# Kernel optimization log

Hardware: AMD Instinct MI355X
Metric: run time of the kernel (lower is better)

Reference implementation:

```python
import jax, jax.numpy as jnp
import numpy as np

B, R, N, D, H, QK, K = 32, 200, 200, 128, 8, 16, 10
CLIP = 10.0  # standard POMO logit clipping


def setup_inputs() -> dict:
    key = jax.random.key(0)
    ks = jax.random.split(key, 12)
    encoded_nodes = jax.random.normal(ks[0], (B, N, D), jnp.float32)
    distance = jax.random.uniform(ks[1], (B, N, N), jnp.float32)
    current = jax.random.randint(ks[2], (B, R), 0, N)
    u = jax.random.uniform(ks[3], (B, R, N))
    ninf_mask = jnp.where(u < 0.3, -jnp.inf, 0.0).astype(jnp.float32)
    s = 0.02
    Wq = jax.random.normal(ks[4], (2 * D, H * QK), jnp.float32) * s
    Wk = jax.random.normal(ks[5], (D, H * QK), jnp.float32) * s
    Wv = jax.random.normal(ks[6], (D, H * QK), jnp.float32) * s
    Wmhc = jax.random.normal(ks[7], (H * QK, D), jnp.float32) * s
    b_mhc = jnp.zeros((D,), jnp.float32)
    W1 = jax.random.normal(ks[8], (K * D, 5 * D), jnp.float32) * s
    b1 = jnp.zeros((5 * D,), jnp.float32)
    W2 = jax.random.normal(ks[9], (5 * D, D), jnp.float32) * s
    b2 = jnp.zeros((D,), jnp.float32)
    return {"encoded_nodes": encoded_nodes, "distance": distance, "ninf_mask": ninf_mask,
            "current": current, "Wq": Wq, "Wk": Wk, "Wv": Wv, "Wmhc": Wmhc, "b_mhc": b_mhc,
            "W1": W1, "b1": b1, "W2": W2, "b2": b2}


def _search_unvisited(current, distance, ninf_mask):
    # rows of distance at current nodes: [B,R,N] (avoids B*R*N*N materialization)
    dist_f = jnp.take_along_axis(distance, current[:, :, None], axis=1)
    dist_m = jnp.where(jnp.isfinite(ninf_mask), dist_f, jnp.inf)
    neg_vals, idx = jax.lax.top_k(-dist_m, K)  # k smallest distances
    vals = -neg_vals
    return jnp.where(jnp.isinf(vals), N, idx)  # pad index N for masked-out slots


def _gather_pad0(encoded_nodes, idx):
    padded = jnp.concatenate([encoded_nodes, jnp.zeros((B, 1, D), encoded_nodes.dtype)], axis=1)
    g = jnp.take_along_axis(padded, idx.reshape(B, R * K)[:, :, None], axis=1)
    return g.reshape(B, R, K, D)


def _gather_pad_avg(a):
    # replace all-zero (pad) rows by the mean of non-zero rows within each [K,D] group
    is_zero = jnp.sum(a, axis=-1) == 0  # [B,R,K]
    cnt = jnp.maximum(jnp.sum(~is_zero, axis=-1).astype(a.dtype), 1e-9)  # [B,R]
    mean = jnp.sum(a, axis=2) / cnt[..., None]  # [B,R,D]
    return jnp.where(is_zero[..., None], mean[:, :, None, :], a)


def reference(encoded_nodes, distance, ninf_mask, current,
              Wq, Wk, Wv, Wmhc, b_mhc, W1, b1, W2, b2):
    knn = _search_unvisited(current, distance, ninf_mask)         # [B,R,K]
    a = _gather_pad0(encoded_nodes, knn)                          # [B,R,K,D]
    b = _gather_pad_avg(a)                                        # [B,R,K,D]
    h = jnp.maximum(b.reshape(B, R, K * D) @ W1 + b1, 0.0)
    unv = h @ W2 + b2                                             # [B,R,D]
    cur_emb = jnp.take_along_axis(encoded_nodes, current[:, :, None], axis=1)  # [B,R,D]
    qin = jnp.concatenate([cur_emb, unv], axis=-1)                # [B,R,2D]
    q = (qin @ Wq).reshape(B, R, H, QK).transpose(0, 2, 1, 3)     # [B,H,R,QK]
    k = (encoded_nodes @ Wk).reshape(B, N, H, QK).transpose(0, 2, 1, 3)
    v = (encoded_nodes @ Wv).reshape(B, N, H, QK).transpose(0, 2, 1, 3)
    score = jnp.einsum('bhrd,bhnd->bhrn', q, k) / jnp.sqrt(jnp.float32(QK))
    score = score + ninf_mask[:, None]                            # [B,H,R,N]
    w = jax.nn.softmax(score, axis=-1)
    out = jnp.einsum('bhrn,bhnd->bhrd', w, v)
    out = out.transpose(0, 2, 1, 3).reshape(B, R, H * QK)
    mh = out @ Wmhc + b_mhc                                       # [B,R,D]
    sh = jnp.einsum('brd,bnd->brn', mh, encoded_nodes) / jnp.sqrt(jnp.float32(D))
    logits = CLIP * jnp.tanh(sh) + ninf_mask
    return jax.nn.softmax(logits, axis=-1)                        # [B,R,N]
```

## Files before the change

kernel.cpp:

```cpp
#include <hip/hip_runtime.h>
#include <hip/hip_bf16.h>
#include <math.h>

#define Bc 32
#define Rc 200
#define Nc 200
#define Dc 128
#define Hc 8
#define QKc 16
#define Kc 10
#define BRc (Bc*Rc)

typedef __attribute__((ext_vector_type(8))) short short8;
typedef __attribute__((ext_vector_type(4))) float f32x4;
typedef unsigned long long u64;

#define GLOAD_LDS16(g, l) __builtin_amdgcn_global_load_lds( \
    (const __attribute__((address_space(1))) void*)(g), \
    (__attribute__((address_space(3))) void*)(l), 16, 0, 0)

__device__ inline void transpose_tile(const float* __restrict__ src, int lds_,
                                      __hip_bfloat16* __restrict__ dst, int ldd,
                                      int k0, int n0, float scale)
{
    __shared__ float tile[32][33];
    int tx = threadIdx.x & 31, ty = threadIdx.x >> 5;
    #pragma unroll
    for (int i = ty; i < 32; i += 8)
        tile[i][tx] = src[(size_t)(k0 + i) * lds_ + n0 + tx];
    __syncthreads();
    #pragma unroll
    for (int i = ty; i < 32; i += 8)
        dst[(size_t)(n0 + i) * ldd + k0 + tx] = __float2bfloat16(tile[tx][i] * scale);
}

__global__ __launch_bounds__(256) void prep_knn_kernel(
    const float* __restrict__ W1, const float* __restrict__ W2,
    const float* __restrict__ Wq, const float* __restrict__ Wmhc,
    const float* __restrict__ Wk, const float* __restrict__ Wv,
    const float* __restrict__ b2, const float* __restrict__ enc,
    const float* __restrict__ dist, const float* __restrict__ mask,
    const int* __restrict__ cur,
    __hip_bfloat16* __restrict__ W1t, __hip_bfloat16* __restrict__ Wkvt,
    __hip_bfloat16* __restrict__ Wmb, __hip_bfloat16* __restrict__ Wcat,
    float* __restrict__ bq, __hip_bfloat16* __restrict__ encb,
    unsigned* __restrict__ aoff, __hip_bfloat16* __restrict__ hq,
    u64* __restrict__ maskbits)
{
    int bid = blockIdx.x;
    int t = threadIdx.x;
    if (bid < 800) {
        transpose_tile(W1, 640, W1t, 1280, (bid % 40) * 32, (bid / 40) * 32, 1.f);
    } else if (bid < 816) {
        int id = bid - 800;
        transpose_tile(Wk, 128, Wkvt, 128, (id & 3) * 32, (id >> 2) * 32, 1.f);
    } else if (bid < 832) {
        int id = bid - 816;
        transpose_tile(Wv, 128, Wkvt + 128 * 128, 128, (id & 3) * 32, (id >> 2) * 32, 1.f);
    } else if (bid < 848) {
        int e = (bid - 832) * 1024 + t * 4;
        #pragma unroll
        for (int j = 0; j < 4; ++j) Wmb[e + j] = __float2bfloat16(Wmhc[e + j]);
    } else if (bid < 864) {
        int id = bid - 848;
        transpose_tile(Wq, 128, Wcat, 768, (id & 3) * 32, (id >> 2) * 32, 0.25f);
    } else if (bid < 904) {
        int j0 = (bid - 864) * 16;
        int n = t & 127, half = t >> 7;
        #pragma unroll
        for (int jj = 0; jj < 8; ++jj) {
            int j = j0 + half * 8 + jj;
            float acc = 0.f;
            for (int k = 0; k < 128; ++k)
                acc = fmaf(W2[(size_t)j * 128 + k], Wq[(size_t)(128 + k) * 128 + n], acc);
            Wcat[(size_t)n * 768 + 128 + j] = __float2bfloat16(acc * 0.25f);
        }
    } else if (bid < 929) {
        size_t base = (size_t)(bid - 904) * 32768 + (size_t)t * 4;
        #pragma unroll 4
        for (int it = 0; it < 32; ++it) {
            size_t i = base + (size_t)it * 1024;
            float4 v = *(const float4*)(enc + i);
            encb[i + 0] = __float2bfloat16(v.x);
            encb[i + 1] = __float2bfloat16(v.y);
            encb[i + 2] = __float2bfloat16(v.z);
            encb[i + 3] = __float2bfloat16(v.w);
        }
    } else if (bid == 929) {
        if (t < 128) {
            float acc = 0.f;
            for (int k = 0; k < 128; ++k)
                acc = fmaf(b2[k], Wq[(size_t)(128 + k) * 128 + t], acc);
            bq[t] = acc * 0.25f;
        }
    } else {
        int lane = t & 63, w = t >> 6;
        int br = (bid - 930) * 4 + w;
        int b = br / Rc;
        int c = cur[br];
        const float* drow = dist + ((size_t)b * Nc + c) * Nc;
        const float* mrow = mask + (size_t)br * Nc;

        float v[4];
        #pragma unroll
        for (int j = 0; j < 4; ++j) {
            int n = lane + 64 * j;
            bool allowed = false;
            float val = INFINITY;
            if (n < Nc) {
                float mv = mrow[n];
                if (!isinf(mv)) { val = drow[n]; allowed = true; }
            }
            v[j] = val;
            u64 wb = __ballot(allowed);
            if (lane == 0) maskbits[(size_t)br * 4 + j] = wb;
        }
        int idxs[Kc];
        unsigned myrow = 0;
        #pragma unroll
        for (int k = 0; k < Kc; ++k) {
            float bv = v[0]; int bn = lane;
            #pragma unroll
            for (int j = 1; j < 4; ++j) {
                if (v[j] < bv) { bv = v[j]; bn = lane + 64 * j; }
            }
            #pragma unroll
            for (int off = 32; off > 0; off >>= 1) {
                float ov = __shfl_xor(bv, off);
                int   on = __shfl_xor(bn, off);
                if (ov < bv || (ov == bv && on < bn)) { bv = ov; bn = on; }
            }
            bool pad = isinf(bv);
            idxs[k] = pad ? Nc : bn;
            if (lane == k) myrow = pad ? (unsigned)(Bc * Nc + br) : (unsigned)(b * Nc + bn);
            int oj = bn >> 6, ol = bn & 63;
            if (!pad && lane == ol) v[oj] = INFINITY;
        }
        if (lane < Kc) aoff[(size_t)br * 16 + lane] = myrow << 7;

        const float* erow = enc + ((size_t)b * Nc + c) * Dc;
        __hip_bfloat16* hrow = hq + (size_t)br * 768;
        hrow[lane]      = __float2bfloat16(erow[lane]);
        hrow[lane + 64] = __float2bfloat16(erow[lane + 64]);

        if (idxs[Kc - 1] == Nc) {
            float cnt = 0.f;
            #pragma unroll
            for (int k = 0; k < Kc; ++k) cnt += (idxs[k] < Nc) ? 1.f : 0.f;
            float icnt = 1.f / fmaxf(cnt, 1e-9f);
            #pragma unroll
            for (int half = 0; half < 2; ++half) {
                int d = lane + 64 * half;
                float sum = 0.f;
                #pragma unroll
                for (int k = 0; k < Kc; ++k) {
                    if (idxs[k] < Nc)
                        sum += enc[((size_t)b * Nc + idxs[k]) * Dc + d];
                }
                encb[((size_t)(Bc * Nc) + br) * Dc + d] = __float2bfloat16(sum * icnt);
            }
        }
    }
}

__global__ __launch_bounds__(256) void fused_gemms_kernel(
    const __hip_bfloat16* __restrict__ encb, const unsigned* __restrict__ aoff,
    const __hip_bfloat16* __restrict__ W1t, const float* __restrict__ b1,
    const __hip_bfloat16* __restrict__ Wkvt, const __hip_bfloat16* __restrict__ Wmb,
    const float* __restrict__ bmhc, const float* __restrict__ enc,
    __hip_bfloat16* __restrict__ hq, __hip_bfloat16* __restrict__ kvf,
    __hip_bfloat16* __restrict__ em, float* __restrict__ be)
{
    __shared__ short Asl[4][64 * 32];
    __shared__ short Bsl[4][64 * 32];
    int bid = blockIdx.x;
    int tid = threadIdx.x;
    int wave = tid >> 6, lane = tid & 63;
    int lrow = lane >> 2;
    int cg   = lane & 3;
    int ss   = (lane >> 3) & 3;
    int gq   = (cg - ss) & 3;
    int wm = wave >> 1, wn = wave & 1;
    int rrow = lane & 15, quad = lane >> 4;
    int srd  = (rrow >> 1) & 3;
    int strip = (wave & 1) * 32;

    if (bid < 1000) {
        int m0 = (bid / 10) * 64, n0 = (bid % 10) * 64;
        unsigned o0[Kc], o1[Kc];
        if (wave < 2) {
            const unsigned* ap0 = aoff + (size_t)(m0 + strip + lrow) * 16;
            const unsigned* ap1 = ap0 + 16 * 16;
            #pragma unroll
            for (int j = 0; j < Kc; ++j) { o0[j] = ap0[j]; o1[j] = ap1[j]; }
        }
        const short* Eb = (const short*)encb;
        const short* gB0 = (const short*)W1t + (size_t)(n0 + strip + lrow) * 1280 + gq * 8;
        const short* gB1 = gB0 + (size_t)16 * 1280;

        f32x4 acc[2][2];
        #pragma unroll
        for (int i = 0; i < 2; ++i)
            #pragma unroll
            for (int j = 0; j < 2; ++j)
                acc[i][j] = (f32x4){0.f, 0.f, 0.f, 0.f};

        #pragma unroll
        for (int kt = 0; kt < 10; ++kt) {
            __syncthreads();
            #pragma unroll
            for (int s = 0; s < 4; ++s) {
                if (wave < 2) {
                    GLOAD_LDS16(Eb + o0[kt] + s * 32 + gq * 8, &Asl[s][strip * 32]);
                    GLOAD_LDS16(Eb + o1[kt] + s * 32 + gq * 8, &Asl[s][(strip + 16) * 32]);
                } else {
                    GLOAD_LDS16(gB0 + kt * 128 + s * 32, &Bsl[s][strip * 32]);
                    GLOAD_LDS16(gB1 + kt * 128 + s * 32, &Bsl[s][(strip + 16) * 32]);
                }
            }
            __syncthreads();
            #pragma unroll
            for (int s = 0; s < 4; ++s) {
                short8 afr[2], bfr[2];
                #pragma unroll
                for (int mt = 0; mt < 2; ++mt)
                    afr[mt] = *(const short8*)&Asl[s][(wm * 32 + mt * 16 + rrow) * 32 + ((quad + srd) & 3) * 8];
                #pragma unroll
                for (int nt = 0; nt < 2; ++nt)
                    bfr[nt] = *(const short8*)&Bsl[s][(wn * 32 + nt * 16 + rrow) * 32 + ((quad + srd) & 3) * 8];
                #pragma unroll
                for (int mt = 0; mt < 2; ++mt)
                    #pragma unroll
                    for (int nt = 0; nt < 2; ++nt)
                        acc[mt][nt] = __builtin_amdgcn_mfma_f32_16x16x32_bf16(
                            afr[mt], bfr[nt], acc[mt][nt], 0, 0, 0);
            }
        }
        #pragma unroll
        for (int mt = 0; mt < 2; ++mt)
            #pragma unroll
            for (int nt = 0; nt < 2; ++nt) {
                int n = wn * 32 + nt * 16 + rrow;
                float bv = b1[n0 + n];
                #pragma unroll
                for (int i = 0; i < 4; ++i) {
                    int m = m0 + wm * 32 + mt * 16 + quad * 4 + i;
                    float vv = fmaxf(acc[mt][nt][i] + bv, 0.f);
                    hq[(size_t)m * 768 + 128 + n0 + n] = __float2bfloat16(vv);
                }
            }
    } else if (bid < 1600) {
        const short* Bbase; __hip_bfloat16* Cout; int ldc, m0, n0;
        if (bid < 1400) {
            int id = bid - 1000;
            Bbase = (const short*)Wkvt; Cout = kvf; ldc = 256;
            m0 = (id >> 2) * 64; n0 = (id & 3) * 64;
        } else {
            int id = bid - 1400;
            Bbase = (const short*)Wmb; Cout = em; ldc = 128;
            m0 = (id >> 1) * 64; n0 = (id & 1) * 64;
        }
        const short* g0 = (wave < 2)
            ? (const short*)encb + (size_t)(m0 + strip + lrow) * 128 + gq * 8
            : Bbase + (size_t)(n0 + strip + lrow) * 128 + gq * 8;
        const short* g1 = g0 + (size_t)16 * 128;

        f32x4 acc[2][2];
        #pragma unroll
        for (int i = 0; i < 2; ++i)
            #pragma unroll
            for (int j = 0; j < 2; ++j)
                acc[i][j] = (f32x4){0.f, 0.f, 0.f, 0.f};

        #pragma unroll
        for (int s = 0; s < 4; ++s) {
            short* l0 = (wave < 2) ? &Asl[s][strip * 32] : &Bsl[s][strip * 32];
            short* l1 = (wave < 2) ? &Asl[s][(strip + 16) * 32] : &Bsl[s][(strip + 16) * 32];
            GLOAD_LDS16(g0 + s * 32, l0);
            GLOAD_LDS16(g1 + s * 32, l1);
        }
        __syncthreads();
        #pragma unroll
        for (int s = 0; s < 4; ++s) {
            short8 afr[2], bfr[2];
            #pragma unroll
            for (int mt = 0; mt < 2; ++mt)
                afr[mt] = *(const short8*)&Asl[s][(wm * 32 + mt * 16 + rrow) * 32 + ((quad + srd) & 3) * 8];
            #pragma unroll
            for (int nt = 0; nt < 2; ++nt)
                bfr[nt] = *(const short8*)&Bsl[s][(wn * 32 + nt * 16 + rrow) * 32 + ((quad + srd) & 3) * 8];
            #pragma unroll
            for (int mt = 0; mt < 2; ++mt)
                #pragma unroll
                for (int nt = 0; nt < 2; ++nt)
                    acc[mt][nt] = __builtin_amdgcn_mfma_f32_16x16x32_bf16(
                        afr[mt], bfr[nt], acc[mt][nt], 0, 0, 0);
        }
        #pragma unroll
        for (int mt = 0; mt < 2; ++mt)
            #pragma unroll
            for (int nt = 0; nt < 2; ++nt) {
                int n = wn * 32 + nt * 16 + rrow;
                #pragma unroll
                for (int i = 0; i < 4; ++i) {
                    int m = m0 + wm * 32 + mt * 16 + quad * 4 + i;
                    Cout[(size_t)m * ldc + n0 + n] = __float2bfloat16(acc[mt][nt][i]);
                }
            }
    } else {
        int i = (bid - 1600) * 256 + tid;
        if (i < Bc * Nc) {
            const float* row = enc + (size_t)i * 128;
            float acc = 0.f;
            #pragma unroll
            for (int dq = 0; dq < 32; ++dq) {
                float4 e4 = *(const float4*)(row + dq * 4);
                acc = fmaf(bmhc[dq * 4 + 0], e4.x, acc);
                acc = fmaf(bmhc[dq * 4 + 1], e4.y, acc);
                acc = fmaf(bmhc[dq * 4 + 2], e4.z, acc);
                acc = fmaf(bmhc[dq * 4 + 3], e4.w, acc);
            }
            be[i] = acc;
        }
    }
}

__global__ __launch_bounds__(256) void qgemm_kernel(
    const __hip_bfloat16* __restrict__ hq, const __hip_bfloat16* __restrict__ Wcat,
    const float* __restrict__ bq, __hip_bfloat16* __restrict__ q)
{
    __shared__ short Asl[4][64 * 32];
    __shared__ short Bsl[4][64 * 32];
    int tid = threadIdx.x;
    int wave = tid >> 6, lane = tid & 63;
    int m0 = blockIdx.y * 64, n0 = blockIdx.x * 64;
    int lrow = lane >> 2;
    int cg   = lane & 3;
    int ss   = (lane >> 3) & 3;
    int gq   = (cg - ss) & 3;
    int wm = wave >> 1, wn = wave & 1;
    int rrow = lane & 15, quad = lane >> 4;
    int srd  = (rrow >> 1) & 3;
    int strip = (wave & 1) * 32;

    const short* g0 = (wave < 2)
        ? (const short*)hq + (size_t)(m0 + strip + lrow) * 768 + gq * 8
        : (const short*)Wcat + (size_t)(n0 + strip + lrow) * 768 + gq * 8;
    const short* g1 = g0 + (size_t)16 * 768;

    f32x4 acc[2][2];
    #pragma unroll
    for (int i = 0; i < 2; ++i)
        #pragma unroll
        for (int j = 0; j < 2; ++j)
            acc[i][j] = (f32x4){0.f, 0.f, 0.f, 0.f};

    for (int k0 = 0; k0 < 768; k0 += 128) {
        __syncthreads();
        #pragma unroll
        for (int s = 0; s < 4; ++s) {
            short* l0 = (wave < 2) ? &Asl[s][strip * 32] : &Bsl[s][strip * 32];
            short* l1 = (wave < 2) ? &Asl[s][(strip + 16) * 32] : &Bsl[s][(strip + 16) * 32];
            GLOAD_LDS16(g0 + k0 + s * 32, l0);
            GLOAD_LDS16(g1 + k0 + s * 32, l1);
        }
        __syncthreads();
        #pragma unroll
        for (int s = 0; s < 4; ++s) {
            short8 afr[2], bfr[2];
            #pragma unroll
            for (int mt = 0; mt < 2; ++mt)
                afr[mt] = *(const short8*)&Asl[s][(wm * 32 + mt * 16 + rrow) * 32 + ((quad + srd) & 3) * 8];
            #pragma unroll
            for (int nt = 0; nt < 2; ++nt)
                bfr[nt] = *(const short8*)&Bsl[s][(wn * 32 + nt * 16 + rrow) * 32 + ((quad + srd) & 3) * 8];
            #pragma unroll
            for (int mt = 0; mt < 2; ++mt)
                #pragma unroll
                for (int nt = 0; nt < 2; ++nt)
                    acc[mt][nt] = __builtin_amdgcn_mfma_f32_16x16x32_bf16(
                        afr[mt], bfr[nt], acc[mt][nt], 0, 0, 0);
        }
    }

    #pragma unroll
    for (int mt = 0; mt < 2; ++mt) {
        #pragma unroll
        for (int nt = 0; nt < 2; ++nt) {
            int n = wn * 32 + nt * 16 + rrow;
            float bv = bq[n0 + n];
            #pragma unroll
            for (int i = 0; i < 4; ++i) {
                int m = m0 + wm * 32 + mt * 16 + quad * 4 + i;
                q[(size_t)m * 128 + n0 + n] = __float2bfloat16(acc[mt][nt][i] + bv);
            }
        }
    }
}

__global__ __launch_bounds__(256) void attn_mfma_kernel(
    const __hip_bfloat16* __restrict__ q, const __hip_bfloat16* __restrict__ kvf,
    const u64* __restrict__ maskbits, __hip_bfloat16* __restrict__ att)
{
    constexpr int RP = 208;
    constexpr int QS = 40;
    constexpr int VS = 232;
    __shared__ short Qs[RP * QS];
    __shared__ short Ks[RP * QS];
    __shared__ short Vt[16 * VS];
    __shared__ short Ps[4][16 * VS];
    __shared__ u64 smask[RP][4];

    int b = blockIdx.x >> 3, h = blockIdx.x & 7;
    int half = blockIdx.y;
    int t = threadIdx.x;
    int wave = t >> 6, lane = t & 63;
    int rrow = lane & 15, quad = lane >> 4;

    const short8 z8 = {0, 0, 0, 0, 0, 0, 0, 0};
    for (int idx = t; idx < RP * 2; idx += 256) {
        int r = idx >> 1, g = idx & 1;
        short8 qa = z8, ka = z8;
        if (r < Rc) {
            qa = *(const short8*)((const short*)q + ((size_t)(b * Rc + r)) * 128 + h * 16 + g * 8);
            ka = *(const short8*)((const short*)kvf + ((size_t)(b * Nc + r)) * 256 + h * 16 + g * 8);
        }
        *(short8*)&Qs[r * QS + g * 8] = qa;
        *(short8*)&Ks[r * QS + g * 8] = ka;
        *(short8*)&Qs[r * QS + 16 + g * 8] = z8;
        *(short8*)&Ks[r * QS + 16 + g * 8] = z8;
    }
    if (t < Rc) {
        const short* vp = (const short*)kvf + ((size_t)(b * Nc + t)) * 256 + 128 + h * 16;
        short8 v0 = *(const short8*)vp;
        short8 v1 = *(const short8*)(vp + 8);
        #pragma unroll
        for (int d = 0; d < 8; ++d) Vt[d * VS + t] = v0[d];
        #pragma unroll
        for (int d = 0; d < 8; ++d) Vt[(d + 8) * VS + t] = v1[d];
    }
    for (int idx = t; idx < 16 * 32; idx += 256) {
        int d = idx >> 5, cN = 200 + (idx & 31);
        if (cN < VS) Vt[d * VS + cN] = 0;
    }
    for (int idx = lane; idx < 16 * 16; idx += 64) {
        int rr = idx >> 4, cc = 208 + (idx & 15);
        Ps[wave][rr * VS + cc] = 0;
    }
    for (int idx = t; idx < RP * 4; idx += 256) {
        int r = idx >> 2, w = idx & 3;
        smask[r][w] = (r < Rc) ? maskbits[((size_t)b * Rc + r) * 4 + w] : ~0ull;
    }
    __syncthreads();

    int rt0 = half * 7, rt1 = half ? 13 : 7;
    for (int rt = rt0 + wave; rt < rt1; rt += 4) {
        short8 qf = *(const short8*)&Qs[(rt * 16 + rrow) * QS + quad * 8];
        f32x4 sacc[13];
        #pragma unroll
        for (int nt = 0; nt < 13; ++nt) {
            short8 kf = *(const short8*)&Ks[(nt * 16 + rrow) * QS + quad * 8];
            sacc[nt] = __builtin_amdgcn_mfma_f32_16x16x32_bf16(
                qf, kf, (f32x4){0.f, 0.f, 0.f, 0.f}, 0, 0, 0);
        }
        float inv[4];
        #pragma unroll
        for (int i = 0; i < 4; ++i) {
            int r = rt * 16 + quad * 4 + i;
            u64 wv0 = smask[r][0], wv1 = smask[r][1], wv2 = smask[r][2], wv3 = smask[r][3];
            float mx = -INFINITY;
            #pragma unroll
            for (int nt = 0; nt < 13; ++nt) {
                u64 w = (nt < 4) ? wv0 : (nt < 8) ? wv1 : (nt < 12) ? wv2 : wv3;
                int sh = ((nt & 3) << 4) + rrow;
                float s = ((w >> sh) & 1ull) ? sacc[nt][i] : -INFINITY;
                sacc[nt][i] = s;
                mx = fmaxf(mx, s);
            }
            mx = fmaxf(mx, __shfl_xor(mx, 1));
            mx = fmaxf(mx, __shfl_xor(mx, 2));
            mx = fmaxf(mx, __shfl_xor(mx, 4));
            mx = fmaxf(mx, __shfl_xor(mx, 8));
            float l = 0.f;
            #pragma unroll
            for (int nt = 0; nt < 13; ++nt) {
                float p = __expf(sacc[nt][i] - mx);
                sacc[nt][i] = p;
                l += p;
            }
            l += __shfl_xor(l, 1);
            l += __shfl_xor(l, 2);
            l += __shfl_xor(l, 4);
            l += __shfl_xor(l, 8);
            inv[i] = (l > 0.f) ? 1.f / l : 0.f;
        }
        #pragma unroll
        for (int nt = 0; nt < 13; ++nt)
            #pragma unroll
            for (int i = 0; i < 4; ++i)
                *(__hip_bfloat16*)&Ps[wave][(quad * 4 + i) * VS + nt * 16 + rrow] =
                    __float2bfloat16(sacc[nt][i]);
        f32x4 oacc = (f32x4){0.f, 0.f, 0.f, 0.f};
        #pragma unroll
        for (int kt = 0; kt < 7; ++kt) {
            short8 pf = *(const short8*)&Ps[wave][rrow * VS + kt * 32 + quad * 8];
            short8 vf = *(const short8*)&Vt[rrow * VS + kt * 32 + quad * 8];
            oacc = __builtin_amdgcn_mfma_f32_16x16x32_bf16(pf, vf, oacc, 0, 0, 0);
        }
        #pragma unroll
        for (int i = 0; i < 4; ++i) {
            int r = rt * 16 + quad * 4 + i;
            if (r < Rc)
                att[((size_t)(b * Rc + r)) * 128 + h * 16 + rrow] =
                    __float2bfloat16(oacc[i] * inv[i]);
        }
    }
}

__global__ __launch_bounds__(128) void logits_softmax_kernel(
    const __hip_bfloat16* __restrict__ att, const __hip_bfloat16* __restrict__ em,
    const float* __restrict__ be, const u64* __restrict__ maskbits,
    float* __restrict__ out)
{
    __shared__ short Asl[4][32 * 32];
    __shared__ short Bsl[4][208 * 32];
    __shared__ u64 sm[32][4];
    __shared__ float sbe[208];
    int b = blockIdx.x, m0 = blockIdx.y * 32;
    int t = threadIdx.x, wave = t >> 6, lane = t & 63;
    int lrow = lane >> 2, cg = lane & 3, ss = (lane >> 3) & 3, gq = (cg - ss) & 3;
    int rrow = lane & 15, quad = lane >> 4, srd = (rrow >> 1) & 3;

    const short* Aa = (const short*)att + ((size_t)b * Rc + m0) * 128;
    const short* Ben = (const short*)em + (size_t)b * Nc * 128;

    #pragma unroll
    for (int kc = 0; kc < 4; ++kc)
        GLOAD_LDS16(Aa + (size_t)(wave * 16 + lrow) * 128 + kc * 32 + gq * 8,
                    &Asl[kc][(wave * 16) * 32]);
    for (int cch = wave; cch < 13; cch += 2)
        #pragma unroll
        for (int kc = 0; kc < 4; ++kc)
            GLOAD_LDS16(Ben + (size_t)(cch * 16 + lrow) * 128 + kc * 32 + gq * 8,
                        &Bsl[kc][(cch * 16) * 32]);
    {
        int r = t >> 2, w = t & 3;
        sm[r][w] = (m0 + r < Rc) ? maskbits[((size_t)b * Rc + m0 + r) * 4 + w] : 0ull;
    }
    for (int i = t; i < 208; i += 128) sbe[i] = (i < Nc) ? be[(size_t)b * Nc + i] : 0.f;
    __syncthreads();

    short8 afr[4];
    #pragma unroll
    for (int kc = 0; kc < 4; ++kc)
        afr[kc] = *(const short8*)&Asl[kc][(wave * 16 + rrow) * 32 + ((quad + srd) & 3) * 8];

    f32x4 acc[13];
    #pragma unroll
    for (int nt = 0; nt < 13; ++nt)
        acc[nt] = (f32x4){0.f, 0.f, 0.f, 0.f};
    #pragma unroll
    for (int nt = 0; nt < 13; ++nt)
        #pragma unroll
        for (int kc = 0; kc < 4; ++kc) {
            short8 bfr = *(const short8*)
                &Bsl[kc][(nt * 16 + rrow) * 32 + ((quad + srd) & 3) * 8];
            acc[nt] = __builtin_amdgcn_mfma_f32_16x16x32_bf16(afr[kc], bfr, acc[nt], 0, 0, 0);
        }

    const float scale = 0.08838834764831843f;
    #pragma unroll
    for (int i = 0; i < 4; ++i) {
        int rloc = wave * 16 + quad * 4 + i;
        int r = m0 + rloc;
        u64 w0 = sm[rloc][0], w1 = sm[rloc][1], w2 = sm[rloc][2], w3 = sm[rloc][3];
        float vals[13];
        float mx = -INFINITY;
        #pragma unroll
        for (int nt = 0; nt < 13; ++nt) {
            u64 w = (nt < 4) ? w0 : (nt < 8) ? w1 : (nt < 12) ? w2 : w3;
            int sh = ((nt & 3) << 4) + rrow;
            float lg = ((w >> sh) & 1ull)
                     ? 10.f * tanhf((acc[nt][i] + sbe[nt * 16 + rrow]) * scale)
                     : -INFINITY;
            vals[nt] = lg;
            mx = fmaxf(mx, lg);
        }
        mx = fmaxf(mx, __shfl_xor(mx, 1));
        mx = fmaxf(mx, __shfl_xor(mx, 2));
        mx = fmaxf(mx, __shfl_xor(mx, 4));
        mx = fmaxf(mx, __shfl_xor(mx, 8));
        float l = 0.f;
        #pragma unroll
        for (int nt = 0; nt < 13; ++nt) {
            float p = (vals[nt] == -INFINITY) ? 0.f : __expf(vals[nt] - mx);
            vals[nt] = p;
            l += p;
        }
        l += __shfl_xor(l, 1);
        l += __shfl_xor(l, 2);
        l += __shfl_xor(l, 4);
        l += __shfl_xor(l, 8);
        float inv = (l > 0.f) ? 1.f / l : 0.f;
        if (r < Rc) {
            #pragma unroll
            for (int nt = 0; nt < 13; ++nt) {
                int n = nt * 16 + rrow;
                if (n < Nc)
                    out[((size_t)b * Rc + r) * Nc + n] = vals[nt] * inv;
            }
        }
    }
}

extern "C" void kernel_launch(void* const* d_in, const int* in_sizes, int n_in,
                              void* d_out, int out_size, void* d_ws, size_t ws_size,
                              hipStream_t stream)
{
    const float* enc  = (const float*)d_in[0];
    const float* dist = (const float*)d_in[1];
    const float* mask = (const float*)d_in[2];
    const int*   cur  = (const int*)d_in[3];
    const float* Wq   = (const float*)d_in[4];
    const float* Wk   = (const float*)d_in[5];
    const float* Wv   = (const float*)d_in[6];
    const float* Wmhc = (const float*)d_in[7];
    const float* bmhc = (const float*)d_in[8];
    const float* W1   = (const float*)d_in[9];
    const float* b1   = (const float*)d_in[10];
    const float* W2   = (const float*)d_in[11];
    const float* b2   = (const float*)d_in[12];
    float* out = (float*)d_out;

    char* ws = (char*)d_ws;
    size_t off = 0;
    auto alloc = [&](size_t bytes) { char* p = ws + off; off += (bytes + 255) & ~(size_t)255; return p; };
    __hip_bfloat16* W1t  = (__hip_bfloat16*)alloc((size_t)640 * 1280 * 2);
    __hip_bfloat16* Wkvt = (__hip_bfloat16*)alloc((size_t)256 * 128 * 2);
    __hip_bfloat16* Wmb  = (__hip_bfloat16*)alloc((size_t)128 * 128 * 2);
    __hip_bfloat16* Wcat = (__hip_bfloat16*)alloc((size_t)128 * 768 * 2);
    float* bq = (float*)alloc((size_t)128 * 4);
    __hip_bfloat16* encb = (__hip_bfloat16*)alloc((size_t)(Bc * Nc + BRc + 64) * Dc * 2);
    unsigned* aoff = (unsigned*)alloc((size_t)BRc * 16 * 4);
    __hip_bfloat16* hq   = (__hip_bfloat16*)alloc((size_t)BRc * 768 * 2);
    __hip_bfloat16* q    = (__hip_bfloat16*)alloc((size_t)BRc * 128 * 2);
    __hip_bfloat16* kvf  = (__hip_bfloat16*)alloc((size_t)Bc * Nc * 256 * 2);
    __hip_bfloat16* att  = (__hip_bfloat16*)alloc((size_t)(BRc + 64) * 128 * 2);
    __hip_bfloat16* em   = (__hip_bfloat16*)alloc((size_t)(Bc * Nc + 64) * 128 * 2);
    float* be = (float*)alloc((size_t)Bc * Nc * 4);
    u64* maskbits = (u64*)alloc((size_t)BRc * 4 * 8);

    prep_knn_kernel<<<2530, 256, 0, stream>>>(
        W1, W2, Wq, Wmhc, Wk, Wv, b2, enc, dist, mask, cur,
        W1t, Wkvt, Wmb, Wcat, bq, encb, aoff, hq, maskbits);
    fused_gemms_kernel<<<1625, 256, 0, stream>>>(
        encb, aoff, W1t, b1, Wkvt, Wmb, bmhc, enc, hq, kvf, em, be);
    qgemm_kernel<<<dim3(2, BRc / 64), 256, 0, stream>>>(hq, Wcat, bq, q);
    attn_mfma_kernel<<<dim3(Bc * Hc, 2), 256, 0, stream>>>(q, kvf, maskbits, att);
    logits_softmax_kernel<<<dim3(Bc, 7), 128, 0, stream>>>(att, em, be, maskbits, out);
}
```

Measured before the change: 172.6 us.

## Use 128x128 tiles with double-buffered LDS for the W1 gather GEMM

```diff
diff --git a/kernel.cpp b/kernel.cpp
--- a/kernel.cpp
+++ b/kernel.cpp
@@ -171,8 +171,8 @@
     __hip_bfloat16* __restrict__ hq, __hip_bfloat16* __restrict__ kvf,
     __hip_bfloat16* __restrict__ em, float* __restrict__ be)
 {
-    __shared__ short Asl[4][64 * 32];
-    __shared__ short Bsl[4][64 * 32];
+    __shared__ short Asl[4][128 * 32];
+    __shared__ short Bsl[4][128 * 32];
     int bid = blockIdx.x;
     int tid = threadIdx.x;
     int wave = tid >> 6, lane = tid & 63;
@@ -185,78 +185,93 @@
     int srd  = (rrow >> 1) & 3;
     int strip = (wave & 1) * 32;
 
-    if (bid < 1000) {
-        int m0 = (bid / 10) * 64, n0 = (bid % 10) * 64;
-        unsigned o0[Kc], o1[Kc];
-        if (wave < 2) {
-            const unsigned* ap0 = aoff + (size_t)(m0 + strip + lrow) * 16;
-            const unsigned* ap1 = ap0 + 16 * 16;
-            #pragma unroll
-            for (int j = 0; j < Kc; ++j) { o0[j] = ap0[j]; o1[j] = ap1[j]; }
-        }
-        const short* Eb = (const short*)encb;
-        const short* gB0 = (const short*)W1t + (size_t)(n0 + strip + lrow) * 1280 + gq * 8;
+    if (bid < 250) {
+        int m0 = (bid / 5) * 128, n0 = (bid % 5) * 128;
+
+        unsigned oA0[10], oA1[10];
+        {
+            const unsigned* ap = aoff + (size_t)(m0 + wave * 32 + lrow) * 16;
+            #pragma unroll
+            for (int j = 0; j < 10; ++j) { oA0[j] = ap[j]; oA1[j] = ap[256 + j]; }
+        }
+        const short* Eb  = (const short*)encb;
+        const short* gB0 = (const short*)W1t + (size_t)(n0 + wave * 32 + lrow) * 1280 + gq * 8;
         const short* gB1 = gB0 + (size_t)16 * 1280;
 
-        f32x4 acc[2][2];
-        #pragma unroll
-        for (int i = 0; i < 2; ++i)
-            #pragma unroll
-            for (int j = 0; j < 2; ++j)
+        f32x4 acc[4][4];
+        #pragma unroll
+        for (int i = 0; i < 4; ++i)
+            #pragma unroll
+            for (int j = 0; j < 4; ++j)
                 acc[i][j] = (f32x4){0.f, 0.f, 0.f, 0.f};
 
-        #pragma unroll
-        for (int kt = 0; kt < 10; ++kt) {
+#define G1_STAGE(bsel, kt) do {                                                          \
+            int g_ = (kt) >> 1, hh_ = ((kt) & 1) * 64;                                   \
+            _Pragma("unroll")                                                            \
+            for (int s_ = 0; s_ < 2; ++s_) {                                             \
+                GLOAD_LDS16(Eb + oA0[g_] + hh_ + s_ * 32 + gq * 8,                       \
+                            &Asl[((bsel) << 1) | s_][(wave * 32) * 32]);                 \
+                GLOAD_LDS16(Eb + oA1[g_] + hh_ + s_ * 32 + gq * 8,                       \
+                            &Asl[((bsel) << 1) | s_][(wave * 32 + 16) * 32]);            \
+                GLOAD_LDS16(gB0 + (kt) * 64 + s_ * 32,                                   \
+                            &Bsl[((bsel) << 1) | s_][(wave * 32) * 32]);                 \
+                GLOAD_LDS16(gB1 + (kt) * 64 + s_ * 32,                                   \
+                            &Bsl[((bsel) << 1) | s_][(wave * 32 + 16) * 32]);            \
+            } } while (0)
+
+#define G1_COMPUTE(bsel) do {                                                            \
+            _Pragma("unroll")                                                            \
+            for (int s_ = 0; s_ < 2; ++s_) {                                             \
+                short8 afr[4], bfr[4];                                                   \
+                _Pragma("unroll")                                                        \
+                for (int mt = 0; mt < 4; ++mt)                                           \
+                    afr[mt] = *(const short8*)&Asl[((bsel) << 1) | s_]                   \
+                        [(wm * 64 + mt * 16 + rrow) * 32 + ((quad + srd) & 3) * 8];      \
+                _Pragma("unroll")                                                        \
+                for (int nt = 0; nt < 4; ++nt)                                           \
+                    bfr[nt] = *(const short8*)&Bsl[((bsel) << 1) | s_]                   \
+                        [(wn * 64 + nt * 16 + rrow) * 32 + ((quad + srd) & 3) * 8];      \
+                _Pragma("unroll")                                                        \
+                for (int mt = 0; mt < 4; ++mt)                                           \
+                    _Pragma("unroll")                                                    \
+                    for (int nt = 0; nt < 4; ++nt)                                       \
+                        acc[mt][nt] = __builtin_amdgcn_mfma_f32_16x16x32_bf16(           \
+                            afr[mt], bfr[nt], acc[mt][nt], 0, 0, 0);                     \
+            } } while (0)
+
+        G1_STAGE(0, 0);
+        __syncthreads();
+        #pragma unroll
+        for (int kt = 0; kt < 19; ++kt) {
+            G1_STAGE((kt & 1) ^ 1, kt + 1);
+            G1_COMPUTE(kt & 1);
             __syncthreads();
-            #pragma unroll
-            for (int s = 0; s < 4; ++s) {
-                if (wave < 2) {
-                    GLOAD_LDS16(Eb + o0[kt] + s * 32 + gq * 8, &Asl[s][strip * 32]);
-                    GLOAD_LDS16(Eb + o1[kt] + s * 32 + gq * 8, &Asl[s][(strip + 16) * 32]);
-                } else {
-                    GLOAD_LDS16(gB0 + kt * 128 + s * 32, &Bsl[s][strip * 32]);
-                    GLOAD_LDS16(gB1 + kt * 128 + s * 32, &Bsl[s][(strip + 16) * 32]);
-                }
-            }
-            __syncthreads();
-            #pragma unroll
-            for (int s = 0; s < 4; ++s) {
-                short8 afr[2], bfr[2];
-                #pragma unroll
-                for (int mt = 0; mt < 2; ++mt)
-                    afr[mt] = *(const short8*)&Asl[s][(wm * 32 + mt * 16 + rrow) * 32 + ((quad + srd) & 3) * 8];
-                #pragma unroll
-                for (int nt = 0; nt < 2; ++nt)
-                    bfr[nt] = *(const short8*)&Bsl[s][(wn * 32 + nt * 16 + rrow) * 32 + ((quad + srd) & 3) * 8];
-                #pragma unroll
-                for (int mt = 0; mt < 2; ++mt)
-                    #pragma unroll
-                    for (int nt = 0; nt < 2; ++nt)
-                        acc[mt][nt] = __builtin_amdgcn_mfma_f32_16x16x32_bf16(
-                            afr[mt], bfr[nt], acc[mt][nt], 0, 0, 0);
-            }
-        }
-        #pragma unroll
-        for (int mt = 0; mt < 2; ++mt)
-            #pragma unroll
-            for (int nt = 0; nt < 2; ++nt) {
-                int n = wn * 32 + nt * 16 + rrow;
+        }
+        G1_COMPUTE(1);
+#undef G1_STAGE
+#undef G1_COMPUTE
+
+        #pragma unroll
+        for (int mt = 0; mt < 4; ++mt)
+            #pragma unroll
+            for (int nt = 0; nt < 4; ++nt) {
+                int n = wn * 64 + nt * 16 + rrow;
                 float bv = b1[n0 + n];
                 #pragma unroll
                 for (int i = 0; i < 4; ++i) {
-                    int m = m0 + wm * 32 + mt * 16 + quad * 4 + i;
+                    int m = m0 + wm * 64 + mt * 16 + quad * 4 + i;
                     float vv = fmaxf(acc[mt][nt][i] + bv, 0.f);
                     hq[(size_t)m * 768 + 128 + n0 + n] = __float2bfloat16(vv);
                 }
             }
-    } else if (bid < 1600) {
+    } else if (bid < 850) {
         const short* Bbase; __hip_bfloat16* Cout; int ldc, m0, n0;
-        if (bid < 1400) {
-            int id = bid - 1000;
+        if (bid < 650) {
+            int id = bid - 250;
             Bbase = (const short*)Wkvt; Cout = kvf; ldc = 256;
             m0 = (id >> 2) * 64; n0 = (id & 3) * 64;
         } else {
-            int id = bid - 1400;
+            int id = bid - 650;
             Bbase = (const short*)Wmb; Cout = em; ldc = 128;
             m0 = (id >> 1) * 64; n0 = (id & 1) * 64;
         }
@@ -308,7 +323,7 @@
                 }
             }
     } else {
-        int i = (bid - 1600) * 256 + tid;
+        int i = (bid - 850) * 256 + tid;
         if (i < Bc * Nc) {
             const float* row = enc + (size_t)i * 128;
             float acc = 0.f;
@@ -653,7 +668,7 @@
     prep_knn_kernel<<<2530, 256, 0, stream>>>(
         W1, W2, Wq, Wmhc, Wk, Wv, b2, enc, dist, mask, cur,
         W1t, Wkvt, Wmb, Wcat, bq, encb, aoff, hq, maskbits);
-    fused_gemms_kernel<<<1625, 256, 0, stream>>>(
+    fused_gemms_kernel<<<875, 256, 0, stream>>>(
         encb, aoff, W1t, b1, Wkvt, Wmb, bmhc, enc, hq, kvf, em, be);
     qgemm_kernel<<<dim3(2, BRc / 64), 256, 0, stream>>>(hq, Wcat, bq, q);
     attn_mfma_kernel<<<dim3(Bc * Hc, 2), 256, 0, stream>>>(q, kvf, maskbits, att);
```

Result: slower. 179.2 us (+3.8%).
